# Performance work log

Measured on AMD Instinct MI355X. Metric: run time of the kernel, lower is better.

The kernel has to match this reference:

```python
import jax, jax.numpy as jnp
import numpy as np

B, S, D, H = 2, 2048, 1024, 16
DK = D // H

def setup_inputs() -> dict:
    key = jax.random.key(0)
    ks = jax.random.split(key, 12)
    def lin(k):
        kw, kb = jax.random.split(k)
        bound = 1.0 / np.sqrt(D)
        W = jax.random.uniform(kw, (D, D), jnp.float32, -bound, bound)
        b = jax.random.uniform(kb, (D,), jnp.float32, -bound, bound)
        return W, b
    Wq, bq = lin(ks[0]); Wk, bk = lin(ks[1]); Wv, bv = lin(ks[2]); Wo, bo = lin(ks[3])
    q = jax.random.normal(ks[4], (B, S, D), jnp.float32)
    k = jax.random.normal(ks[5], (B, S, D), jnp.float32)
    v = jax.random.normal(ks[6], (B, S, D), jnp.float32)
    mask = jnp.ones((1, 1, S, S), jnp.int32)
    return {"q": q, "k": k, "v": v, "mask": mask,
            "Wq": Wq, "bq": bq, "Wk": Wk, "bk": bk,
            "Wv": Wv, "bv": bv, "Wo": Wo, "bo": bo}

def reference(q, k, v, mask, Wq, bq, Wk, bk, Wv, bv, Wo, bo):
    # torch Linear: y = x @ W.T + b
    Q = (q @ Wq.T + bq).reshape(B, S, H, DK).transpose(0, 2, 1, 3)  # [B,H,S,DK]
    K = (k @ Wk.T + bk).reshape(B, S, H, DK).transpose(0, 2, 1, 3)
    V = (v @ Wv.T + bv).reshape(B, S, H, DK).transpose(0, 2, 1, 3)
    scores = jnp.einsum('bhqd,bhkd->bhqk', Q, K) / jnp.sqrt(jnp.float32(DK))
    scores = jnp.where(mask == 0, jnp.float32(-1e9), scores)
    attn = jax.nn.softmax(scores, axis=-1)
    context = jnp.einsum('bhqk,bhkd->bhqd', attn, V)  # [B,H,S,DK]
    concat = context.transpose(0, 2, 1, 3).reshape(B, S, D)
    return concat @ Wo.T + bo
```

## Files before the change

kernel.cpp:

```cpp
#include <hip/hip_runtime.h>
#include <hip/hip_bf16.h>

#define BB 2
#define SS 2048
#define DD 1024
#define HH 16
#define DKK 64

typedef __hip_bfloat16 bf16;
typedef unsigned short u16;
using frag_ab = __attribute__((ext_vector_type(8))) short;
using frag_cd = __attribute__((ext_vector_type(4))) float;

__device__ inline u16 f2bf(float f) {
    bf16 h = __float2bfloat16(f);
    return *reinterpret_cast<u16*>(&h);
}

__device__ inline float exp2_hw(float x) {
    float r;
    asm("v_exp_f32 %0, %1" : "=v"(r) : "v"(x));
    return r;
}

__device__ inline unsigned pk2bf(float a, float b) {
    __hip_bfloat162 h = __float22bfloat162_rn(float2{a, b});
    return *reinterpret_cast<unsigned*>(&h);
}

__device__ inline void gld16(const void* g, void* l) {
    __builtin_amdgcn_global_load_lds((const __attribute__((address_space(1))) void*)g,
                                     (__attribute__((address_space(3))) void*)l,
                                     16, 0, 0);
}

__device__ inline int swz16(int idx) {
    return idx ^ (((idx >> 6) & 7) << 3);
}

__global__ __launch_bounds__(256) void prep(
    const float* __restrict__ q, const float* __restrict__ k, const float* __restrict__ v,
    const float* __restrict__ Wq, const float* __restrict__ Wk,
    const float* __restrict__ Wv, const float* __restrict__ Wo,
    u16* __restrict__ qb, u16* __restrict__ kb, u16* __restrict__ vb,
    u16* __restrict__ Wqb, u16* __restrict__ Wkb, u16* __restrict__ Wvb, u16* __restrict__ Wob,
    const int* __restrict__ mask, int* __restrict__ flags) {
    int bid = blockIdx.x;
    int t = threadIdx.x;
    if (bid < 8192) {
        const float* src;
        u16* dst;
        int local;
        if (bid < 6144) {
            int ts = bid >> 11;
            local = bid & 2047;
            src = ts == 0 ? q : (ts == 1 ? k : v);
            dst = ts == 0 ? qb : (ts == 1 ? kb : vb);
        } else {
            int wsel = (bid - 6144) >> 9;
            local = (bid - 6144) & 511;
            src = wsel == 0 ? Wq : (wsel == 1 ? Wk : (wsel == 2 ? Wv : Wo));
            dst = wsel == 0 ? Wqb : (wsel == 1 ? Wkb : (wsel == 2 ? Wvb : Wob));
        }
        size_t base = (size_t)local * 2048 + t * 8;
        float4 a = *(const float4*)&src[base];
        float4 b = *(const float4*)&src[base + 4];
        ushort4 u0, u1;
        u0.x = f2bf(a.x); u0.y = f2bf(a.y); u0.z = f2bf(a.z); u0.w = f2bf(a.w);
        u1.x = f2bf(b.x); u1.y = f2bf(b.y); u1.z = f2bf(b.z); u1.w = f2bf(b.w);
        *(ushort4*)&dst[base] = u0;
        *(ushort4*)&dst[base + 4] = u1;
    } else {
        int tile = bid - 8192;
        int qt = tile >> 5, kt = tile & 31;
        __shared__ int f;
        if (t == 0) f = 0;
        __syncthreads();
        int qq = qt * 64 + (t >> 2);
        const int4* row = (const int4*)(mask + (size_t)qq * SS + kt * 64 + (t & 3) * 16);
        int anyz = 0;
#pragma unroll
        for (int i = 0; i < 4; ++i) {
            int4 m4 = row[i];
            anyz |= (m4.x == 0) | (m4.y == 0) | (m4.z == 0) | (m4.w == 0);
        }
        if (anyz) f = 1;
        __syncthreads();
        if (t == 0) flags[tile] = f;
    }
}

__global__ __launch_bounds__(256) void qkv_gemm(
    const u16* __restrict__ Aq, const u16* __restrict__ Ak, const u16* __restrict__ Av,
    const u16* __restrict__ Wq, const u16* __restrict__ Wk, const u16* __restrict__ Wv,
    const float* __restrict__ bq, const float* __restrict__ bk, const float* __restrict__ bv,
    u16* __restrict__ Qo, u16* __restrict__ Ko, u16* __restrict__ Vo) {
    __shared__ u16 As[128 * 32];
    __shared__ u16 Bs[128 * 32];

    int z = blockIdx.z;
    const u16* A = z == 0 ? Aq : (z == 1 ? Ak : Av);
    const u16* W = z == 0 ? Wq : (z == 1 ? Wk : Wv);
    const float* bias = z == 0 ? bq : (z == 1 ? bk : bv);
    u16* out = z == 0 ? Qo : (z == 1 ? Ko : Vo);

    int t = threadIdx.x;
    int m0 = blockIdx.y * 128;
    int n0 = blockIdx.x * 128;
    int w = t >> 6, lane = t & 63;
    int quad = lane >> 4, l16 = lane & 15;
    int wm = w >> 1, wn = w & 1;

    const u16* Ab = A + (size_t)m0 * DD;
    const u16* Wb = W + (size_t)n0 * DD;

    frag_cd acc[4][4];
#pragma unroll
    for (int mt = 0; mt < 4; ++mt)
#pragma unroll
        for (int nt = 0; nt < 4; ++nt) acc[mt][nt] = frag_cd{0.f, 0.f, 0.f, 0.f};

    for (int k0 = 0; k0 < DD; k0 += 32) {
        if (k0) __syncthreads();
#pragma unroll
        for (int i = 0; i < 2; ++i) {
            int c = t + i * 256;
            int row = c >> 2, kc = (c & 3) * 8;
            gld16(Ab + (size_t)row * DD + k0 + kc, &As[c * 8]);
            gld16(Wb + (size_t)row * DD + k0 + kc, &Bs[c * 8]);
        }
        __syncthreads();

        frag_ab af[4], bfr[4];
#pragma unroll
        for (int mt = 0; mt < 4; ++mt)
            af[mt] = *(const frag_ab*)&As[(wm * 64 + mt * 16 + l16) * 32 + quad * 8];
#pragma unroll
        for (int nt = 0; nt < 4; ++nt)
            bfr[nt] = *(const frag_ab*)&Bs[(wn * 64 + nt * 16 + l16) * 32 + quad * 8];
#pragma unroll
        for (int mt = 0; mt < 4; ++mt)
#pragma unroll
            for (int nt = 0; nt < 4; ++nt)
                acc[mt][nt] = __builtin_amdgcn_mfma_f32_16x16x32_bf16(
                    af[mt], bfr[nt], acc[mt][nt], 0, 0, 0);
    }

    float scale = z == 0 ? 0.18033688f : 1.0f;
#pragma unroll
    for (int nt = 0; nt < 4; ++nt) {
        int n = n0 + wn * 64 + nt * 16 + l16;
        float bv_ = bias[n];
        int h_ = n >> 6, d_ = n & 63;
#pragma unroll
        for (int mt = 0; mt < 4; ++mt) {
            int mb = m0 + wm * 64 + mt * 16 + quad * 4;
            int b_ = mb >> 11, s_ = mb & 2047;
            if (z == 2) {
                ushort4 u;
                u.x = f2bf(acc[mt][nt][0] + bv_);
                u.y = f2bf(acc[mt][nt][1] + bv_);
                u.z = f2bf(acc[mt][nt][2] + bv_);
                u.w = f2bf(acc[mt][nt][3] + bv_);
                *(ushort4*)&out[((size_t)(b_ * HH + h_) * DKK + d_) * SS + s_] = u;
            } else {
#pragma unroll
                for (int r = 0; r < 4; ++r)
                    out[((size_t)(b_ * HH + h_) * SS + s_ + r) * DKK + d_] =
                        f2bf((acc[mt][nt][r] + bv_) * scale);
            }
        }
    }
}

__global__ __launch_bounds__(256) void out_gemm(const u16* __restrict__ A,
                                                const u16* __restrict__ W,
                                                const float* __restrict__ bias,
                                                float* __restrict__ out) {
    __shared__ u16 As[128 * 32];
    __shared__ u16 Bs[64 * 32];

    int t = threadIdx.x;
    int m0 = blockIdx.y * 128;
    int n0 = blockIdx.x * 64;
    int w = t >> 6, lane = t & 63;
    int quad = lane >> 4, l16 = lane & 15;
    int wm = w >> 1, wn = w & 1;

    const u16* Ab = A + (size_t)m0 * DD;
    const u16* Wb = W + (size_t)n0 * DD;

    frag_cd acc[4][2];
#pragma unroll
    for (int mt = 0; mt < 4; ++mt)
#pragma unroll
        for (int nt = 0; nt < 2; ++nt) acc[mt][nt] = frag_cd{0.f, 0.f, 0.f, 0.f};

    for (int k0 = 0; k0 < DD; k0 += 32) {
        if (k0) __syncthreads();
#pragma unroll
        for (int i = 0; i < 2; ++i) {
            int c = t + i * 256;
            int row = c >> 2, kc = (c & 3) * 8;
            gld16(Ab + (size_t)row * DD + k0 + kc, &As[c * 8]);
        }
        {
            int row = t >> 2, kc = (t & 3) * 8;
            gld16(Wb + (size_t)row * DD + k0 + kc, &Bs[t * 8]);
        }
        __syncthreads();

        frag_ab af[4], bfr[2];
#pragma unroll
        for (int mt = 0; mt < 4; ++mt)
            af[mt] = *(const frag_ab*)&As[(wm * 64 + mt * 16 + l16) * 32 + quad * 8];
#pragma unroll
        for (int nt = 0; nt < 2; ++nt)
            bfr[nt] = *(const frag_ab*)&Bs[(wn * 32 + nt * 16 + l16) * 32 + quad * 8];
#pragma unroll
        for (int mt = 0; mt < 4; ++mt)
#pragma unroll
            for (int nt = 0; nt < 2; ++nt)
                acc[mt][nt] = __builtin_amdgcn_mfma_f32_16x16x32_bf16(
                    af[mt], bfr[nt], acc[mt][nt], 0, 0, 0);
    }

#pragma unroll
    for (int nt = 0; nt < 2; ++nt) {
        int n = n0 + wn * 32 + nt * 16 + l16;
        float bv_ = bias[n];
#pragma unroll
        for (int mt = 0; mt < 4; ++mt) {
            int mb = m0 + wm * 64 + mt * 16 + quad * 4;
#pragma unroll
            for (int r = 0; r < 4; ++r)
                out[(size_t)(mb + r) * DD + n] = acc[mt][nt][r] + bv_;
        }
    }
}

__global__ __launch_bounds__(512) void attn_mfma(const u16* __restrict__ Qb,
                                                 const u16* __restrict__ Kb,
                                                 const u16* __restrict__ Vb,
                                                 const int* __restrict__ mask,
                                                 const int* __restrict__ flags,
                                                 u16* __restrict__ C) {
    __shared__ u16 Ks[64 * 64];
    __shared__ u16 Vt[64 * 64];
    __shared__ u16 Pw[8][16 * 72];

    int blk = blockIdx.x;
    int Qt = blk & 15;
    int bh = blk >> 4;
    int h = bh & 15;
    int b = bh >> 4;
    int q0 = Qt * 128;

    const u16* Kg = Kb + (size_t)bh * SS * DKK;
    const u16* Vg = Vb + (size_t)bh * DKK * SS;

    int t = threadIdx.x;
    int w = t >> 6;
    int lane = t & 63;
    int quad = lane >> 4;
    int l16 = lane & 15;

    frag_ab bq0, bq1;
    {
        const u16* Qr = Qb + ((size_t)bh * SS + q0 + w * 16 + l16) * DKK;
        bq0 = *(const frag_ab*)&Qr[quad * 8];
        bq1 = *(const frag_ab*)&Qr[32 + quad * 8];
    }

    frag_ab ones;
#pragma unroll
    for (int j = 0; j < 8; ++j) ones[j] = (short)0x3F80;

    frag_cd o[4];
#pragma unroll
    for (int dt = 0; dt < 4; ++dt) o[dt] = frag_cd{0.f, 0.f, 0.f, 0.f};
    frag_cd lacc = frag_cd{0.f, 0.f, 0.f, 0.f};
    float m_prev = -1e30f;

    int vd = t >> 3;
    int vc = (t & 7) * 8;
    int fbase = (Qt * 2 + (w >> 2)) * 32;

    unsigned azmask = 0;
#pragma unroll
    for (int i = 0; i < 32; ++i) azmask |= (flags[fbase + i] != 0 ? 1u : 0u) << i;

    const int4* kptr = (const int4*)Kg + t;
    const u16*  vptr = Vg + (size_t)vd * SS + vc;

    int4 kr0 = *kptr;
    int4 vr0 = *(const int4*)vptr;

    for (int kt = 0; kt < 32; ++kt) {
        if (kt) __syncthreads();
        *(int4*)&Ks[swz16(8 * t)] = kr0;
        *(int4*)&Vt[swz16(vd * 64 + vc)] = vr0;
        if (kt < 31) {
            kptr += 512;
            vptr += 64;
            kr0 = *kptr;
            vr0 = *(const int4*)vptr;
        }
        __syncthreads();

        float s[4][4];
        __builtin_amdgcn_s_setprio(1);
#pragma unroll
        for (int nt = 0; nt < 4; ++nt) {
            int kr = nt * 16 + l16;
            frag_ab ak0 = *(const frag_ab*)&Ks[swz16(kr * 64 + quad * 8)];
            frag_ab ak1 = *(const frag_ab*)&Ks[swz16(kr * 64 + 32 + quad * 8)];
            frag_cd sf = frag_cd{0.f, 0.f, 0.f, 0.f};
            sf = __builtin_amdgcn_mfma_f32_16x16x32_bf16(ak0, bq0, sf, 0, 0, 0);
            sf = __builtin_amdgcn_mfma_f32_16x16x32_bf16(ak1, bq1, sf, 0, 0, 0);
#pragma unroll
            for (int r = 0; r < 4; ++r) s[nt][r] = sf[r];
        }
        __builtin_amdgcn_s_setprio(0);

        if ((azmask >> kt) & 1) {
            int qg = q0 + w * 16 + l16;
#pragma unroll
            for (int nt = 0; nt < 4; ++nt)
#pragma unroll
                for (int r = 0; r < 4; ++r) {
                    int kg = kt * 64 + nt * 16 + quad * 4 + r;
                    if (mask[(size_t)qg * SS + kg] == 0) s[nt][r] = -1e9f;
                }
        }

        float m0_ = fmaxf(fmaxf(s[0][0], s[0][1]), fmaxf(s[0][2], s[0][3]));
        float m1_ = fmaxf(fmaxf(s[1][0], s[1][1]), fmaxf(s[1][2], s[1][3]));
        float m2_ = fmaxf(fmaxf(s[2][0], s[2][1]), fmaxf(s[2][2], s[2][3]));
        float m3_ = fmaxf(fmaxf(s[3][0], s[3][1]), fmaxf(s[3][2], s[3][3]));
        float mc = fmaxf(fmaxf(m0_, m1_), fmaxf(m2_, m3_));
        mc = fmaxf(mc, __shfl_xor(mc, 16));
        mc = fmaxf(mc, __shfl_xor(mc, 32));
        if (!__all(mc <= m_prev + 11.f)) {
            float mnew = fmaxf(m_prev, mc);
            float alpha = exp2_hw(m_prev - mnew);
#pragma unroll
            for (int r = 0; r < 4; ++r) lacc[r] *= alpha;
#pragma unroll
            for (int dt = 0; dt < 4; ++dt)
#pragma unroll
                for (int r = 0; r < 4; ++r) o[dt][r] *= alpha;
            m_prev = mnew;
        }

        float p[4][4];
#pragma unroll
        for (int nt = 0; nt < 4; ++nt)
#pragma unroll
            for (int r = 0; r < 4; ++r)
                p[nt][r] = exp2_hw(s[nt][r] - m_prev);

#pragma unroll
        for (int nt = 0; nt < 4; ++nt) {
            uint2 up;
            up.x = pk2bf(p[nt][0], p[nt][1]);
            up.y = pk2bf(p[nt][2], p[nt][3]);
            *(uint2*)&Pw[w][l16 * 72 + nt * 16 + quad * 4] = up;
        }
        frag_ab bp0 = *(const frag_ab*)&Pw[w][l16 * 72 + quad * 8];
        frag_ab bp1 = *(const frag_ab*)&Pw[w][l16 * 72 + 32 + quad * 8];

        __builtin_amdgcn_s_setprio(1);
        lacc = __builtin_amdgcn_mfma_f32_16x16x32_bf16(ones, bp0, lacc, 0, 0, 0);
        lacc = __builtin_amdgcn_mfma_f32_16x16x32_bf16(ones, bp1, lacc, 0, 0, 0);
#pragma unroll
        for (int dt = 0; dt < 4; ++dt) {
            int dr = dt * 16 + l16;
            frag_ab av0 = *(const frag_ab*)&Vt[swz16(dr * 64 + quad * 8)];
            frag_ab av1 = *(const frag_ab*)&Vt[swz16(dr * 64 + 32 + quad * 8)];
            o[dt] = __builtin_amdgcn_mfma_f32_16x16x32_bf16(av0, bp0, o[dt], 0, 0, 0);
            o[dt] = __builtin_amdgcn_mfma_f32_16x16x32_bf16(av1, bp1, o[dt], 0, 0, 0);
        }
        __builtin_amdgcn_s_setprio(0);
    }

    {
        float inv = 1.f / lacc[0];
        int qg = q0 + w * 16 + l16;
        u16* Crow = C + ((size_t)b * SS + qg) * DD + h * 64;
#pragma unroll
        for (int dt = 0; dt < 4; ++dt) {
            uint2 u;
            u.x = pk2bf(o[dt][0] * inv, o[dt][1] * inv);
            u.y = pk2bf(o[dt][2] * inv, o[dt][3] * inv);
            *(uint2*)&Crow[dt * 16 + quad * 4] = u;
        }
    }
}

extern "C" void kernel_launch(void* const* d_in, const int* in_sizes, int n_in,
                              void* d_out, int out_size, void* d_ws, size_t ws_size,
                              hipStream_t stream) {
    const float* q = (const float*)d_in[0];
    const float* k = (const float*)d_in[1];
    const float* v = (const float*)d_in[2];
    const int* mask = (const int*)d_in[3];
    const float* Wq = (const float*)d_in[4];
    const float* bq = (const float*)d_in[5];
    const float* Wk = (const float*)d_in[6];
    const float* bk = (const float*)d_in[7];
    const float* Wv = (const float*)d_in[8];
    const float* bv = (const float*)d_in[9];
    const float* Wo = (const float*)d_in[10];
    const float* bo = (const float*)d_in[11];
    float* out = (float*)d_out;

    const size_t MB = 1024u * 1024u;
    char* ws = (char*)d_ws;
    u16* qb = (u16*)(ws + 0 * MB);
    u16* kb = (u16*)(ws + 8 * MB);
    u16* vb = (u16*)(ws + 16 * MB);
    u16* Wqb = (u16*)(ws + 24 * MB);
    u16* Wkb = (u16*)(ws + 26 * MB);
    u16* Wvb = (u16*)(ws + 28 * MB);
    u16* Wob = (u16*)(ws + 30 * MB);
    u16* Qb = (u16*)(ws + 32 * MB);
    u16* Kb = (u16*)(ws + 40 * MB);
    u16* Vb = (u16*)(ws + 48 * MB);
    int* flags = (int*)(ws + 56 * MB);
    u16* Cw = qb;

    prep<<<9216, 256, 0, stream>>>(q, k, v, Wq, Wk, Wv, Wo,
                                   qb, kb, vb, Wqb, Wkb, Wvb, Wob, mask, flags);

    dim3 grid(DD / 128, (BB * SS) / 128, 3);
    qkv_gemm<<<grid, 256, 0, stream>>>(qb, kb, vb, Wqb, Wkb, Wvb,
                                       bq, bk, bv, Qb, Kb, Vb);

    attn_mfma<<<BB * HH * (SS / 128), 512, 0, stream>>>(Qb, Kb, Vb, mask, flags, Cw);

    out_gemm<<<dim3(DD / 64, (BB * SS) / 128), 256, 0, stream>>>(Cw, Wob, bo, out);
}
```

Before: 247.0 us.

## Process two 16-row query groups per wave in attention, halving block size

```diff
diff --git a/kernel.cpp b/kernel.cpp
--- a/kernel.cpp
+++ b/kernel.cpp
@@ -239,7 +239,7 @@
     }
 }
 
-__global__ __launch_bounds__(512) void attn_mfma(const u16* __restrict__ Qb,
+__global__ __launch_bounds__(256) void attn_mfma(const u16* __restrict__ Qb,
                                                  const u16* __restrict__ Kb,
                                                  const u16* __restrict__ Vb,
                                                  const int* __restrict__ mask,
@@ -247,7 +247,7 @@
                                                  u16* __restrict__ C) {
     __shared__ u16 Ks[64 * 64];
     __shared__ u16 Vt[64 * 64];
-    __shared__ u16 Pw[8][16 * 72];
+    __shared__ u16 Pw[4][2][16 * 72];
 
     int blk = blockIdx.x;
     int Qt = blk & 15;
@@ -265,134 +265,161 @@
     int quad = lane >> 4;
     int l16 = lane & 15;
 
-    frag_ab bq0, bq1;
-    {
-        const u16* Qr = Qb + ((size_t)bh * SS + q0 + w * 16 + l16) * DKK;
-        bq0 = *(const frag_ab*)&Qr[quad * 8];
-        bq1 = *(const frag_ab*)&Qr[32 + quad * 8];
+    frag_ab bq[2][2];
+#pragma unroll
+    for (int g = 0; g < 2; ++g) {
+        const u16* Qr = Qb + ((size_t)bh * SS + q0 + w * 32 + g * 16 + l16) * DKK;
+        bq[g][0] = *(const frag_ab*)&Qr[quad * 8];
+        bq[g][1] = *(const frag_ab*)&Qr[32 + quad * 8];
     }
 
     frag_ab ones;
 #pragma unroll
     for (int j = 0; j < 8; ++j) ones[j] = (short)0x3F80;
 
-    frag_cd o[4];
-#pragma unroll
-    for (int dt = 0; dt < 4; ++dt) o[dt] = frag_cd{0.f, 0.f, 0.f, 0.f};
-    frag_cd lacc = frag_cd{0.f, 0.f, 0.f, 0.f};
-    float m_prev = -1e30f;
-
-    int vd = t >> 3;
-    int vc = (t & 7) * 8;
-    int fbase = (Qt * 2 + (w >> 2)) * 32;
+    frag_cd o[2][4];
+    frag_cd lacc[2];
+#pragma unroll
+    for (int g = 0; g < 2; ++g) {
+#pragma unroll
+        for (int dt = 0; dt < 4; ++dt) o[g][dt] = frag_cd{0.f, 0.f, 0.f, 0.f};
+        lacc[g] = frag_cd{0.f, 0.f, 0.f, 0.f};
+    }
+    float m_prev[2] = {-1e30f, -1e30f};
+
+    int vd0 = t >> 3;
+    int vc0 = (t & 7) * 8;
+    int fbase = (Qt * 2 + (w >> 1)) * 32;
 
     unsigned azmask = 0;
 #pragma unroll
     for (int i = 0; i < 32; ++i) azmask |= (flags[fbase + i] != 0 ? 1u : 0u) << i;
 
     const int4* kptr = (const int4*)Kg + t;
-    const u16*  vptr = Vg + (size_t)vd * SS + vc;
-
-    int4 kr0 = *kptr;
-    int4 vr0 = *(const int4*)vptr;
+    const u16*  vptr0 = Vg + (size_t)vd0 * SS + vc0;
+    const u16*  vptr1 = Vg + (size_t)(vd0 + 32) * SS + vc0;
+
+    int4 kr0 = kptr[0];
+    int4 kr1 = kptr[256];
+    int4 vr0 = *(const int4*)vptr0;
+    int4 vr1 = *(const int4*)vptr1;
 
     for (int kt = 0; kt < 32; ++kt) {
         if (kt) __syncthreads();
         *(int4*)&Ks[swz16(8 * t)] = kr0;
-        *(int4*)&Vt[swz16(vd * 64 + vc)] = vr0;
+        *(int4*)&Ks[swz16(8 * (t + 256))] = kr1;
+        *(int4*)&Vt[swz16(vd0 * 64 + vc0)] = vr0;
+        *(int4*)&Vt[swz16((vd0 + 32) * 64 + vc0)] = vr1;
         if (kt < 31) {
             kptr += 512;
-            vptr += 64;
-            kr0 = *kptr;
-            vr0 = *(const int4*)vptr;
+            vptr0 += 64;
+            vptr1 += 64;
+            kr0 = kptr[0];
+            kr1 = kptr[256];
+            vr0 = *(const int4*)vptr0;
+            vr1 = *(const int4*)vptr1;
         }
         __syncthreads();
 
-        float s[4][4];
+        float s[2][4][4];
         __builtin_amdgcn_s_setprio(1);
 #pragma unroll
         for (int nt = 0; nt < 4; ++nt) {
             int kr = nt * 16 + l16;
             frag_ab ak0 = *(const frag_ab*)&Ks[swz16(kr * 64 + quad * 8)];
             frag_ab ak1 = *(const frag_ab*)&Ks[swz16(kr * 64 + 32 + quad * 8)];
-            frag_cd sf = frag_cd{0.f, 0.f, 0.f, 0.f};
-            sf = __builtin_amdgcn_mfma_f32_16x16x32_bf16(ak0, bq0, sf, 0, 0, 0);
-            sf = __builtin_amdgcn_mfma_f32_16x16x32_bf16(ak1, bq1, sf, 0, 0, 0);
-#pragma unroll
-            for (int r = 0; r < 4; ++r) s[nt][r] = sf[r];
+#pragma unroll
+            for (int g = 0; g < 2; ++g) {
+                frag_cd sf = frag_cd{0.f, 0.f, 0.f, 0.f};
+                sf = __builtin_amdgcn_mfma_f32_16x16x32_bf16(ak0, bq[g][0], sf, 0, 0, 0);
+                sf = __builtin_amdgcn_mfma_f32_16x16x32_bf16(ak1, bq[g][1], sf, 0, 0, 0);
+#pragma unroll
+                for (int r = 0; r < 4; ++r) s[g][nt][r] = sf[r];
+            }
         }
         __builtin_amdgcn_s_setprio(0);
 
         if ((azmask >> kt) & 1) {
-            int qg = q0 + w * 16 + l16;
-#pragma unroll
-            for (int nt = 0; nt < 4; ++nt)
-#pragma unroll
-                for (int r = 0; r < 4; ++r) {
-                    int kg = kt * 64 + nt * 16 + quad * 4 + r;
-                    if (mask[(size_t)qg * SS + kg] == 0) s[nt][r] = -1e9f;
-                }
-        }
-
-        float m0_ = fmaxf(fmaxf(s[0][0], s[0][1]), fmaxf(s[0][2], s[0][3]));
-        float m1_ = fmaxf(fmaxf(s[1][0], s[1][1]), fmaxf(s[1][2], s[1][3]));
-        float m2_ = fmaxf(fmaxf(s[2][0], s[2][1]), fmaxf(s[2][2], s[2][3]));
-        float m3_ = fmaxf(fmaxf(s[3][0], s[3][1]), fmaxf(s[3][2], s[3][3]));
-        float mc = fmaxf(fmaxf(m0_, m1_), fmaxf(m2_, m3_));
-        mc = fmaxf(mc, __shfl_xor(mc, 16));
-        mc = fmaxf(mc, __shfl_xor(mc, 32));
-        if (!__all(mc <= m_prev + 11.f)) {
-            float mnew = fmaxf(m_prev, mc);
-            float alpha = exp2_hw(m_prev - mnew);
-#pragma unroll
-            for (int r = 0; r < 4; ++r) lacc[r] *= alpha;
-#pragma unroll
-            for (int dt = 0; dt < 4; ++dt)
-#pragma unroll
-                for (int r = 0; r < 4; ++r) o[dt][r] *= alpha;
-            m_prev = mnew;
-        }
-
-        float p[4][4];
-#pragma unroll
-        for (int nt = 0; nt < 4; ++nt)
-#pragma unroll
-            for (int r = 0; r < 4; ++r)
-                p[nt][r] = exp2_hw(s[nt][r] - m_prev);
-
-#pragma unroll
-        for (int nt = 0; nt < 4; ++nt) {
-            uint2 up;
-            up.x = pk2bf(p[nt][0], p[nt][1]);
-            up.y = pk2bf(p[nt][2], p[nt][3]);
-            *(uint2*)&Pw[w][l16 * 72 + nt * 16 + quad * 4] = up;
-        }
-        frag_ab bp0 = *(const frag_ab*)&Pw[w][l16 * 72 + quad * 8];
-        frag_ab bp1 = *(const frag_ab*)&Pw[w][l16 * 72 + 32 + quad * 8];
+#pragma unroll
+            for (int g = 0; g < 2; ++g) {
+                int qg = q0 + w * 32 + g * 16 + l16;
+#pragma unroll
+                for (int nt = 0; nt < 4; ++nt)
+#pragma unroll
+                    for (int r = 0; r < 4; ++r) {
+                        int kg = kt * 64 + nt * 16 + quad * 4 + r;
+                        if (mask[(size_t)qg * SS + kg] == 0) s[g][nt][r] = -1e9f;
+                    }
+            }
+        }
+
+#pragma unroll
+        for (int g = 0; g < 2; ++g) {
+            float m0_ = fmaxf(fmaxf(s[g][0][0], s[g][0][1]), fmaxf(s[g][0][2], s[g][0][3]));
+            float m1_ = fmaxf(fmaxf(s[g][1][0], s[g][1][1]), fmaxf(s[g][1][2], s[g][1][3]));
+            float m2_ = fmaxf(fmaxf(s[g][2][0], s[g][2][1]), fmaxf(s[g][2][2], s[g][2][3]));
+            float m3_ = fmaxf(fmaxf(s[g][3][0], s[g][3][1]), fmaxf(s[g][3][2], s[g][3][3]));
+            float mc = fmaxf(fmaxf(m0_, m1_), fmaxf(m2_, m3_));
+            mc = fmaxf(mc, __shfl_xor(mc, 16));
+            mc = fmaxf(mc, __shfl_xor(mc, 32));
+            if (!__all(mc <= m_prev[g] + 11.f)) {
+                float mnew = fmaxf(m_prev[g], mc);
+                float alpha = exp2_hw(m_prev[g] - mnew);
+#pragma unroll
+                for (int r = 0; r < 4; ++r) lacc[g][r] *= alpha;
+#pragma unroll
+                for (int dt = 0; dt < 4; ++dt)
+#pragma unroll
+                    for (int r = 0; r < 4; ++r) o[g][dt][r] *= alpha;
+                m_prev[g] = mnew;
+            }
+
+#pragma unroll
+            for (int nt = 0; nt < 4; ++nt) {
+                uint2 up;
+                up.x = pk2bf(exp2_hw(s[g][nt][0] - m_prev[g]), exp2_hw(s[g][nt][1] - m_prev[g]));
+                up.y = pk2bf(exp2_hw(s[g][nt][2] - m_prev[g]), exp2_hw(s[g][nt][3] - m_prev[g]));
+                *(uint2*)&Pw[w][g][l16 * 72 + nt * 16 + quad * 4] = up;
+            }
+        }
+
+        frag_ab bp[2][2];
+#pragma unroll
+        for (int g = 0; g < 2; ++g) {
+            bp[g][0] = *(const frag_ab*)&Pw[w][g][l16 * 72 + quad * 8];
+            bp[g][1] = *(const frag_ab*)&Pw[w][g][l16 * 72 + 32 + quad * 8];
+        }
 
         __builtin_amdgcn_s_setprio(1);
-        lacc = __builtin_amdgcn_mfma_f32_16x16x32_bf16(ones, bp0, lacc, 0, 0, 0);
-        lacc = __builtin_amdgcn_mfma_f32_16x16x32_bf16(ones, bp1, lacc, 0, 0, 0);
+#pragma unroll
+        for (int g = 0; g < 2; ++g) {
+            lacc[g] = __builtin_amdgcn_mfma_f32_16x16x32_bf16(ones, bp[g][0], lacc[g], 0, 0, 0);
+            lacc[g] = __builtin_amdgcn_mfma_f32_16x16x32_bf16(ones, bp[g][1], lacc[g], 0, 0, 0);
+        }
 #pragma unroll
         for (int dt = 0; dt < 4; ++dt) {
             int dr = dt * 16 + l16;
             frag_ab av0 = *(const frag_ab*)&Vt[swz16(dr * 64 + quad * 8)];
             frag_ab av1 = *(const frag_ab*)&Vt[swz16(dr * 64 + 32 + quad * 8)];
-            o[dt] = __builtin_amdgcn_mfma_f32_16x16x32_bf16(av0, bp0, o[dt], 0, 0, 0);
-            o[dt] = __builtin_amdgcn_mfma_f32_16x16x32_bf16(av1, bp1, o[dt], 0, 0, 0);
+#pragma unroll
+            for (int g = 0; g < 2; ++g) {
+                o[g][dt] = __builtin_amdgcn_mfma_f32_16x16x32_bf16(av0, bp[g][0], o[g][dt], 0, 0, 0);
+                o[g][dt] = __builtin_amdgcn_mfma_f32_16x16x32_bf16(av1, bp[g][1], o[g][dt], 0, 0, 0);
+            }
         }
         __builtin_amdgcn_s_setprio(0);
     }
 
-    {
-        float inv = 1.f / lacc[0];
-        int qg = q0 + w * 16 + l16;
+#pragma unroll
+    for (int g = 0; g < 2; ++g) {
+        float inv = 1.f / lacc[g][0];
+        int qg = q0 + w * 32 + g * 16 + l16;
         u16* Crow = C + ((size_t)b * SS + qg) * DD + h * 64;
 #pragma unroll
         for (int dt = 0; dt < 4; ++dt) {
             uint2 u;
-            u.x = pk2bf(o[dt][0] * inv, o[dt][1] * inv);
-            u.y = pk2bf(o[dt][2] * inv, o[dt][3] * inv);
+            u.x = pk2bf(o[g][dt][0] * inv, o[g][dt][1] * inv);
+            u.y = pk2bf(o[g][dt][2] * inv, o[g][dt][3] * inv);
             *(uint2*)&Crow[dt * 16 + quad * 4] = u;
         }
     }
@@ -437,7 +464,7 @@
     qkv_gemm<<<grid, 256, 0, stream>>>(qb, kb, vb, Wqb, Wkb, Wvb,
                                        bq, bk, bv, Qb, Kb, Vb);
 
-    attn_mfma<<<BB * HH * (SS / 128), 512, 0, stream>>>(Qb, Kb, Vb, mask, flags, Cw);
+    attn_mfma<<<BB * HH * (SS / 128), 256, 0, stream>>>(Qb, Kb, Vb, mask, flags, Cw);
 
     out_gemm<<<dim3(DD / 64, (BB * SS) / 128), 256, 0, stream>>>(Cw, Wob, bo, out);
 }
```

Result: no change. 251.8 us (+1.9%).
